# Optimization experiments

Measured on AMD Instinct MI355X. Metric: run time of the kernel, lower is better.

Reference implementation:

```python
import math
import jax, jax.numpy as jnp
import numpy as np

B, T, C, H = 4, 2048, 1024, 16
D = C // H  # head dim = 64


def setup_inputs() -> dict:
    key = jax.random.key(0)
    ks = jax.random.split(key, 5)
    s = 0.02  # trunc_normal-like init scale
    return {
        "x":  jax.random.normal(ks[0], (B, T, C), dtype=jnp.float32),
        "wq": jax.random.normal(ks[1], (C, C), dtype=jnp.float32) * s,
        "bq": jnp.zeros((C,), dtype=jnp.float32),
        "wk": jax.random.normal(ks[2], (C, C), dtype=jnp.float32) * s,
        "bk": jnp.zeros((C,), dtype=jnp.float32),
        "wv": jax.random.normal(ks[3], (C, C), dtype=jnp.float32) * s,
        "bv": jnp.zeros((C,), dtype=jnp.float32),
        "wp": jax.random.normal(ks[4], (C, C), dtype=jnp.float32) * s,
        "bp": jnp.zeros((C,), dtype=jnp.float32),
    }


def reference(x, wq, bq, wk, bk, wv, bv, wp, bp):
    b, t, c = x.shape
    # QKV projections -> (B, H, T, D)
    q = (x @ wq + bq).reshape(b, t, H, D).transpose(0, 2, 1, 3)
    k = (x @ wk + bk).reshape(b, t, H, D).transpose(0, 2, 1, 3)
    v = (x @ wv + bv).reshape(b, t, H, D).transpose(0, 2, 1, 3)
    present = jnp.stack((k, v))  # (2, B, H, T, D)
    # scaled dot-product with causal mask (layer_past is None path)
    att = jnp.einsum('bhqd,bhkd->bhqk', q, k) * (1.0 / math.sqrt(D))
    causal = jnp.tril(jnp.ones((t, t), dtype=bool))  # (T, T)
    att = jnp.where(causal[None, None], att, -jnp.inf)
    att = jax.nn.softmax(att, axis=-1)
    # dropout prob = 0.0 (eval) -> identity
    y = jnp.einsum('bhqk,bhkd->bhqd', att, v)
    y = y.transpose(0, 2, 1, 3).reshape(b, t, c)
    y = y @ wp + bp
    return (y, present)
```

## Files before the change

### kernel.cpp

```cpp
#include <hip/hip_runtime.h>
#include <hip/hip_bf16.h>
#include <stdint.h>

typedef unsigned short u16;
typedef __bf16 bf16x8 __attribute__((ext_vector_type(8)));
typedef __bf16 bf16x4 __attribute__((ext_vector_type(4)));
typedef float f32x4 __attribute__((ext_vector_type(4)));

#define BB 4
#define TT 2048
#define CC 1024
#define HH 16
#define DD 64

#define QSCALE 0.18033688011112042f

__device__ __forceinline__ u16 f2bf(float f) {
  union { float f; unsigned int u; } v; v.f = f;
  unsigned int u = v.u;
  unsigned int r = (u + 0x7fffu + ((u >> 16) & 1u)) >> 16;
  return (u16)r;
}

__device__ __forceinline__ void async_copy16(const void* g, void* l) {
  __builtin_amdgcn_global_load_lds(
      (const __attribute__((address_space(1))) void*)g,
      (__attribute__((address_space(3))) void*)l, 16, 0, 0);
}

__global__ __launch_bounds__(256) void k_cast_x(const float* __restrict__ x,
                                                u16* __restrict__ xb) {
  int i = (blockIdx.x * 256 + threadIdx.x) * 4;
  float4 f = *reinterpret_cast<const float4*>(x + i);
  ushort4 o;
  o.x = f2bf(f.x); o.y = f2bf(f.y); o.z = f2bf(f.z); o.w = f2bf(f.w);
  *reinterpret_cast<ushort4*>(xb + i) = o;
}

__global__ __launch_bounds__(256) void k_transpose_w(
    const float* __restrict__ w0, const float* __restrict__ w1,
    const float* __restrict__ w2, const float* __restrict__ w3,
    u16* __restrict__ t0, u16* __restrict__ t1,
    u16* __restrict__ t2, u16* __restrict__ t3) {
  const float* w = blockIdx.z == 0 ? w0 : blockIdx.z == 1 ? w1 : blockIdx.z == 2 ? w2 : w3;
  u16* t = blockIdx.z == 0 ? t0 : blockIdx.z == 1 ? t1 : blockIdx.z == 2 ? t2 : t3;
  __shared__ u16 tile[32][33];
  int tx = threadIdx.x, ty = threadIdx.y;
  int k0 = blockIdx.x * 32, n0 = blockIdx.y * 32;
#pragma unroll
  for (int r = 0; r < 4; r++)
    tile[ty + r * 8][tx] = f2bf(w[(size_t)(k0 + ty + r * 8) * CC + n0 + tx]);
  __syncthreads();
#pragma unroll
  for (int r = 0; r < 4; r++)
    t[(size_t)(n0 + ty + r * 8) * CC + k0 + tx] = tile[tx][ty + r * 8];
}

__global__ __launch_bounds__(256) void k_transpose_v(
    const float* __restrict__ out_v, u16* __restrict__ vbt) {
  int tb = blockIdx.x * 64;
  int bh = blockIdx.y;
  const float* src = out_v + (size_t)bh * TT * DD;
  u16* dst = vbt + (size_t)bh * TT * DD;
  __shared__ u16 tile[64][65];
  int tid = threadIdx.x;
#pragma unroll
  for (int p = 0; p < 4; p++) {
    int c = p * 256 + tid;
    int t = c >> 4, d0 = (c & 15) * 4;
    float4 f = *reinterpret_cast<const float4*>(src + (size_t)(tb + t) * DD + d0);
    tile[t][d0 + 0] = f2bf(f.x);
    tile[t][d0 + 1] = f2bf(f.y);
    tile[t][d0 + 2] = f2bf(f.z);
    tile[t][d0 + 3] = f2bf(f.w);
  }
  __syncthreads();
#pragma unroll
  for (int p = 0; p < 2; p++) {
    int c = p * 256 + tid;
    int d = c >> 3, t0 = (c & 7) * 8;
    ushort4 lo, hi;
    lo.x = tile[t0 + 0][d]; lo.y = tile[t0 + 1][d];
    lo.z = tile[t0 + 2][d]; lo.w = tile[t0 + 3][d];
    hi.x = tile[t0 + 4][d]; hi.y = tile[t0 + 5][d];
    hi.z = tile[t0 + 6][d]; hi.w = tile[t0 + 7][d];
    u16* o = dst + (size_t)d * TT + tb + t0;
    *reinterpret_cast<ushort4*>(o) = lo;
    *reinterpret_cast<ushort4*>(o + 4) = hi;
  }
}

#define GEMM_PROLOGUE()                                                        \
  int tid = threadIdx.x;                                                       \
  int lane = tid & 63;                                                         \
  int wave = tid >> 6;                                                         \
  int l15 = lane & 15, quad = lane >> 4;                                       \
  int wave_m = wave & 1, wave_n = wave >> 1;                                   \
  __shared__ u16 lA[3][128 * 32];                                              \
  __shared__ u16 lB[3][128 * 32];                                              \
  f32x4 acc[4][4] = {};                                                        \
  int s_c0 = tid, s_c1 = tid + 256;                                            \
  int s_r0 = s_c0 >> 2, s_e0 = ((s_c0 & 3) ^ ((s_c0 >> 3) & 3)) * 8;           \
  int s_r1 = s_c1 >> 2, s_e1 = ((s_c1 & 3) ^ ((s_c1 >> 3) & 3)) * 8;           \
  auto gstage = [&](int buf, int k0) {                                         \
    async_copy16(A + (size_t)(tile_m + s_r0) * CC + k0 + s_e0,                 \
                 &lA[buf][s_c0 * 8]);                                          \
    async_copy16(A + (size_t)(tile_m + s_r1) * CC + k0 + s_e1,                 \
                 &lA[buf][s_c1 * 8]);                                          \
    async_copy16(Bt + (size_t)(tile_n + s_r0) * CC + k0 + s_e0,                \
                 &lB[buf][s_c0 * 8]);                                          \
    async_copy16(Bt + (size_t)(tile_n + s_r1) * CC + k0 + s_e1,                \
                 &lB[buf][s_c1 * 8]);                                          \
  };                                                                           \
  int offA[4], offB[4];                                                        \
  _Pragma("unroll")                                                            \
  for (int i = 0; i < 4; i++) {                                                \
    int rA = wave_m * 64 + i * 16 + l15;                                       \
    offA[i] = rA * 32 + (quad ^ ((rA >> 1) & 3)) * 8;                          \
    int rB = wave_n * 64 + i * 16 + l15;                                       \
    offB[i] = rB * 32 + (quad ^ ((rB >> 1) & 3)) * 8;                          \
  }                                                                            \
  gstage(0, 0);                                                                \
  gstage(1, 32);                                                               \
  int curb = 0;                                                                \
  for (int ks = 0; ks < CC / 32; ks++) {                                       \
    int nxt = curb + 2; nxt = (nxt >= 3) ? nxt - 3 : nxt;                      \
    if (ks < CC / 32 - 2) {                                                    \
      gstage(nxt, (ks + 2) * 32);                                              \
      asm volatile("s_waitcnt vmcnt(8)" ::: "memory");                         \
    } else if (ks == CC / 32 - 2) {                                            \
      asm volatile("s_waitcnt vmcnt(4)" ::: "memory");                         \
    } else {                                                                   \
      asm volatile("s_waitcnt vmcnt(0)" ::: "memory");                         \
    }                                                                          \
    __builtin_amdgcn_sched_barrier(0);                                         \
    __builtin_amdgcn_s_barrier();                                              \
    __builtin_amdgcn_sched_barrier(0);                                         \
    bf16x8 af[4], bfr[4];                                                      \
    _Pragma("unroll")                                                          \
    for (int i = 0; i < 4; i++)                                                \
      af[i] = *reinterpret_cast<const bf16x8*>(&lA[curb][offA[i]]);            \
    _Pragma("unroll")                                                          \
    for (int j = 0; j < 4; j++)                                                \
      bfr[j] = *reinterpret_cast<const bf16x8*>(&lB[curb][offB[j]]);           \
    __builtin_amdgcn_s_setprio(1);                                             \
    _Pragma("unroll")                                                          \
    for (int i = 0; i < 4; i++)                                                \
      _Pragma("unroll")                                                        \
      for (int j = 0; j < 4; j++)                                              \
        acc[i][j] =                                                            \
            __builtin_amdgcn_mfma_f32_16x16x32_bf16(af[i], bfr[j], acc[i][j],  \
                                                    0, 0, 0);                  \
    __builtin_amdgcn_s_setprio(0);                                             \
    __builtin_amdgcn_sched_barrier(0);                                         \
    __builtin_amdgcn_s_barrier();                                              \
    curb = (curb == 2) ? 0 : curb + 1;                                         \
  }

__global__ __launch_bounds__(256) void k_gemm_qkv(
    const u16* __restrict__ xb,
    const u16* __restrict__ wtq, const u16* __restrict__ wtk, const u16* __restrict__ wtv,
    const float* __restrict__ bq, const float* __restrict__ bk, const float* __restrict__ bv,
    u16* __restrict__ qb, u16* __restrict__ kb,
    float* __restrict__ out_k, float* __restrict__ out_v) {
  int mat = blockIdx.z;
  const u16* A = xb;
  const u16* Bt = mat == 0 ? wtq : mat == 1 ? wtk : wtv;
  const float* bias = mat == 0 ? bq : mat == 1 ? bk : bv;
  int tile_m = blockIdx.x * 128;
  int tile_n = blockIdx.y * 128;

  GEMM_PROLOGUE()

#pragma unroll
  for (int j = 0; j < 4; j++) {
    int n = tile_n + wave_n * 64 + j * 16 + l15;
    int h = n >> 6, d = n & 63;
    float bias_n = bias[n];
#pragma unroll
    for (int i = 0; i < 4; i++) {
#pragma unroll
      for (int r = 0; r < 4; r++) {
        int m = tile_m + wave_m * 64 + i * 16 + quad * 4 + r;
        int b = m >> 11, t = m & 2047;
        float val = acc[i][j][r] + bias_n;
        size_t idx = (((size_t)(b * HH + h)) * TT + t) * DD + d;
        if (mat == 0) {
          qb[idx] = f2bf(val * QSCALE);
        } else if (mat == 1) {
          out_k[idx] = val;
          kb[idx] = f2bf(val);
        } else {
          out_v[idx] = val;
        }
      }
    }
  }
}

__global__ __launch_bounds__(256) void k_gemm_proj(
    const u16* __restrict__ yb, const u16* __restrict__ wtp,
    const float* __restrict__ bp, float* __restrict__ out) {
  const u16* A = yb;
  const u16* Bt = wtp;
  int tile_m = blockIdx.x * 128;
  int tile_n = blockIdx.y * 128;

  GEMM_PROLOGUE()

#pragma unroll
  for (int j = 0; j < 4; j++) {
    int n = tile_n + wave_n * 64 + j * 16 + l15;
    float bias_n = bp[n];
#pragma unroll
    for (int i = 0; i < 4; i++) {
#pragma unroll
      for (int r = 0; r < 4; r++) {
        int m = tile_m + wave_m * 64 + i * 16 + quad * 4 + r;
        out[(size_t)m * CC + n] = acc[i][j][r] + bias_n;
      }
    }
  }
}

__global__ __launch_bounds__(256) void k_attn(
    const u16* __restrict__ qb, const u16* __restrict__ kbuf,
    const u16* __restrict__ vtb, u16* __restrict__ yatt) {
  int qpair = blockIdx.x;
  int bh = blockIdx.y;
  int tid = threadIdx.x;
  int lane = tid & 63;
  int wave = tid >> 6;
  int l15 = lane & 15, quad = lane >> 4;

  const u16* Q = qb + (size_t)bh * TT * DD;
  const u16* K = kbuf + (size_t)bh * TT * DD;
  const u16* Vt = vtb + (size_t)bh * TT * DD;

  __shared__ u16 kl[2][64 * 64];
  __shared__ u16 vl[2][64 * 64];
  __shared__ u16 pl[4][16 * 64];
  u16* plw = pl[wave];

  int h = bh & 15, b = bh >> 4;

  int c0 = tid, c1 = tid + 256;
  int r0 = c0 >> 3, e0 = (((c0 & 7) * 16) ^ ((r0 & 7) << 4)) >> 1;
  int r1 = c1 >> 3, e1 = (((c1 & 7) * 16) ^ ((r1 & 7) << 4)) >> 1;

  auto stage = [&](int buf, int kb0) {
    async_copy16(K + (size_t)(kb0 + r0) * DD + e0, &kl[buf][c0 * 8]);
    async_copy16(K + (size_t)(kb0 + r1) * DD + e1, &kl[buf][c1 * 8]);
    async_copy16(Vt + (size_t)r0 * TT + kb0 + e0, &vl[buf][c0 * 8]);
    async_copy16(Vt + (size_t)r1 * TT + kb0 + e1, &vl[buf][c1 * 8]);
  };

  u16* prow = plw + l15 * 64;
  int xrp = (l15 & 7) << 4;
  int q8 = quad << 3;

#pragma unroll
  for (int side = 0; side < 2; side++) {
    int qt = side == 0 ? qpair : 31 - qpair;

    int qr = qt * 64 + wave * 16 + l15;
    bf16x8 qf0 = *reinterpret_cast<const bf16x8*>(Q + (size_t)qr * DD + quad * 8);
    bf16x8 qf1 = *reinterpret_cast<const bf16x8*>(Q + (size_t)qr * DD + 32 + quad * 8);

    f32x4 o_acc[4] = {};
    float m_run = -1e30f, l_run = 0.f;

    stage(0, 0);

    for (int kblk = 0; kblk <= qt; kblk++) {
      int cur = kblk & 1;
      if (kblk < qt) {
        stage(cur ^ 1, (kblk + 1) * 64);
        asm volatile("s_waitcnt vmcnt(4)" ::: "memory");
      } else {
        asm volatile("s_waitcnt vmcnt(0)" ::: "memory");
      }
      __builtin_amdgcn_sched_barrier(0);
      __builtin_amdgcn_s_barrier();
      __builtin_amdgcn_sched_barrier(0);

      f32x4 s_acc[4];
      __builtin_amdgcn_s_setprio(1);
#pragma unroll
      for (int nb = 0; nb < 4; nb++) {
        int krow = nb * 16 + l15;
        int xr = (krow & 7) << 4;
        const u16* kp = &kl[cur][krow * 64];
        bf16x8 kf0 = *reinterpret_cast<const bf16x8*>(kp + (((quad * 16) ^ xr) >> 1));
        bf16x8 kf1 = *reinterpret_cast<const bf16x8*>(kp + (((64 + quad * 16) ^ xr) >> 1));
        f32x4 z = {};
        z = __builtin_amdgcn_mfma_f32_16x16x32_bf16(kf0, qf0, z, 0, 0, 0);
        z = __builtin_amdgcn_mfma_f32_16x16x32_bf16(kf1, qf1, z, 0, 0, 0);
        s_acc[nb] = z;
      }
      __builtin_amdgcn_s_setprio(0);

      float mx = -1e30f;
      if (kblk == qt) {
        int qg = wave * 16 + l15;
#pragma unroll
        for (int nb = 0; nb < 4; nb++)
#pragma unroll
          for (int r = 0; r < 4; r++) {
            int kg = nb * 16 + quad * 4 + r;
            float s = s_acc[nb][r];
            s = (kg <= qg) ? s : -1e30f;
            s_acc[nb][r] = s;
            mx = fmaxf(mx, s);
          }
      } else {
#pragma unroll
        for (int nb = 0; nb < 4; nb++)
#pragma unroll
          for (int r = 0; r < 4; r++) mx = fmaxf(mx, s_acc[nb][r]);
      }
      mx = fmaxf(mx, __shfl_xor(mx, 16, 64));
      mx = fmaxf(mx, __shfl_xor(mx, 32, 64));

      if (!__all(mx - m_run <= 8.0f)) {
        float mnew = fmaxf(m_run, mx);
        float alpha = __builtin_amdgcn_exp2f(m_run - mnew);
        m_run = mnew;
        l_run *= alpha;
        float av[4];
#pragma unroll
        for (int r = 0; r < 4; r++) av[r] = __shfl(alpha, quad * 4 + r, 64);
#pragma unroll
        for (int db = 0; db < 4; db++)
#pragma unroll
          for (int r = 0; r < 4; r++) o_acc[db][r] *= av[r];
      }

      float sum = 0.f;
#pragma unroll
      for (int nb = 0; nb < 4; nb++)
#pragma unroll
        for (int r = 0; r < 4; r++) {
          float e = __builtin_amdgcn_exp2f(s_acc[nb][r] - m_run);
          s_acc[nb][r] = e;
          sum += e;
        }
      sum += __shfl_xor(sum, 16, 64);
      sum += __shfl_xor(sum, 32, 64);
      l_run += sum;

#pragma unroll
      for (int nb = 0; nb < 4; nb++) {
        bf16x4 pk = {(__bf16)s_acc[nb][0], (__bf16)s_acc[nb][1],
                     (__bf16)s_acc[nb][2], (__bf16)s_acc[nb][3]};
        *reinterpret_cast<bf16x4*>(prow + ((((nb << 5) + q8) ^ xrp) >> 1)) = pk;
      }

      __builtin_amdgcn_s_setprio(1);
#pragma unroll
      for (int half = 0; half < 2; half++) {
        bf16x8 pf = *reinterpret_cast<const bf16x8*>(
            prow + (((half * 64 + quad * 16) ^ xrp) >> 1));
#pragma unroll
        for (int db = 0; db < 4; db++) {
          int vrow = db * 16 + l15;
          bf16x8 vf = *reinterpret_cast<const bf16x8*>(
              &vl[cur][vrow * 64] + (((half * 64 + quad * 16) ^ ((vrow & 7) << 4)) >> 1));
          o_acc[db] = __builtin_amdgcn_mfma_f32_16x16x32_bf16(pf, vf, o_acc[db], 0, 0, 0);
        }
      }
      __builtin_amdgcn_s_setprio(0);

      __builtin_amdgcn_sched_barrier(0);
      __builtin_amdgcn_s_barrier();
    }

    float lr[4];
#pragma unroll
    for (int r = 0; r < 4; r++) lr[r] = __shfl(l_run, quad * 4 + r, 64);
#pragma unroll
    for (int r = 0; r < 4; r++) {
      float inv = 1.0f / lr[r];
      int tq = qt * 64 + wave * 16 + quad * 4 + r;
#pragma unroll
      for (int db = 0; db < 4; db++) {
        int d = db * 16 + l15;
        yatt[((size_t)(b * TT + tq)) * CC + h * DD + d] = f2bf(o_acc[db][r] * inv);
      }
    }
  }
}

extern "C" void kernel_launch(void* const* d_in, const int* in_sizes, int n_in,
                              void* d_out, int out_size, void* d_ws, size_t ws_size,
                              hipStream_t stream) {
  const float* x  = (const float*)d_in[0];
  const float* wq = (const float*)d_in[1];
  const float* bq = (const float*)d_in[2];
  const float* wk = (const float*)d_in[3];
  const float* bk = (const float*)d_in[4];
  const float* wv = (const float*)d_in[5];
  const float* bv = (const float*)d_in[6];
  const float* wp = (const float*)d_in[7];
  const float* bp = (const float*)d_in[8];

  float* out_y = (float*)d_out;
  float* out_k = out_y + (size_t)BB * TT * CC;
  float* out_v = out_k + (size_t)BB * HH * TT * DD;

  u16* xb  = (u16*)d_ws;
  u16* wtq = xb + (size_t)BB * TT * CC;
  u16* wtk = wtq + (size_t)CC * CC;
  u16* wtv = wtk + (size_t)CC * CC;
  u16* wtp = wtv + (size_t)CC * CC;
  u16* qb  = wtp + (size_t)CC * CC;
  u16* kb  = qb + (size_t)BB * TT * CC;
  u16* vbt = kb + (size_t)BB * TT * CC;
  u16* yb  = vbt + (size_t)BB * TT * CC;

  k_cast_x<<<(BB * TT * CC) / 1024, 256, 0, stream>>>(x, xb);
  k_transpose_w<<<dim3(CC / 32, CC / 32, 4), dim3(32, 8), 0, stream>>>(
      wq, wk, wv, wp, wtq, wtk, wtv, wtp);
  k_gemm_qkv<<<dim3(BB * TT / 128, CC / 128, 3), 256, 0, stream>>>(
      xb, wtq, wtk, wtv, bq, bk, bv, qb, kb, out_k, out_v);
  k_transpose_v<<<dim3(TT / 64, BB * HH), 256, 0, stream>>>(out_v, vbt);
  k_attn<<<dim3(16, BB * HH), 256, 0, stream>>>(qb, kb, vbt, yb);
  k_gemm_proj<<<dim3(BB * TT / 128, CC / 128), 256, 0, stream>>>(yb, wtp, bp, out_y);
}
```

Measured before the change: 339.6 us.

## Fuse x cast with weight transpose and write transposed V in QKV epilogue

New measurement: 345.0 us. About the same (+1.6%).

```diff
diff --git a/kernel.cpp b/kernel.cpp
--- a/kernel.cpp
+++ b/kernel.cpp
@@ -28,65 +28,34 @@
       (__attribute__((address_space(3))) void*)l, 16, 0, 0);
 }
 
-__global__ __launch_bounds__(256) void k_cast_x(const float* __restrict__ x,
-                                                u16* __restrict__ xb) {
-  int i = (blockIdx.x * 256 + threadIdx.x) * 4;
-  float4 f = *reinterpret_cast<const float4*>(x + i);
-  ushort4 o;
-  o.x = f2bf(f.x); o.y = f2bf(f.y); o.z = f2bf(f.z); o.w = f2bf(f.w);
-  *reinterpret_cast<ushort4*>(xb + i) = o;
-}
-
-__global__ __launch_bounds__(256) void k_transpose_w(
+__global__ __launch_bounds__(256) void k_prep(
+    const float* __restrict__ x, u16* __restrict__ xb,
     const float* __restrict__ w0, const float* __restrict__ w1,
     const float* __restrict__ w2, const float* __restrict__ w3,
     u16* __restrict__ t0, u16* __restrict__ t1,
     u16* __restrict__ t2, u16* __restrict__ t3) {
-  const float* w = blockIdx.z == 0 ? w0 : blockIdx.z == 1 ? w1 : blockIdx.z == 2 ? w2 : w3;
-  u16* t = blockIdx.z == 0 ? t0 : blockIdx.z == 1 ? t1 : blockIdx.z == 2 ? t2 : t3;
-  __shared__ u16 tile[32][33];
+  int z = blockIdx.z;
   int tx = threadIdx.x, ty = threadIdx.y;
-  int k0 = blockIdx.x * 32, n0 = blockIdx.y * 32;
-#pragma unroll
-  for (int r = 0; r < 4; r++)
-    tile[ty + r * 8][tx] = f2bf(w[(size_t)(k0 + ty + r * 8) * CC + n0 + tx]);
-  __syncthreads();
-#pragma unroll
-  for (int r = 0; r < 4; r++)
-    t[(size_t)(n0 + ty + r * 8) * CC + k0 + tx] = tile[tx][ty + r * 8];
-}
-
-__global__ __launch_bounds__(256) void k_transpose_v(
-    const float* __restrict__ out_v, u16* __restrict__ vbt) {
-  int tb = blockIdx.x * 64;
-  int bh = blockIdx.y;
-  const float* src = out_v + (size_t)bh * TT * DD;
-  u16* dst = vbt + (size_t)bh * TT * DD;
-  __shared__ u16 tile[64][65];
-  int tid = threadIdx.x;
-#pragma unroll
-  for (int p = 0; p < 4; p++) {
-    int c = p * 256 + tid;
-    int t = c >> 4, d0 = (c & 15) * 4;
-    float4 f = *reinterpret_cast<const float4*>(src + (size_t)(tb + t) * DD + d0);
-    tile[t][d0 + 0] = f2bf(f.x);
-    tile[t][d0 + 1] = f2bf(f.y);
-    tile[t][d0 + 2] = f2bf(f.z);
-    tile[t][d0 + 3] = f2bf(f.w);
-  }
-  __syncthreads();
-#pragma unroll
-  for (int p = 0; p < 2; p++) {
-    int c = p * 256 + tid;
-    int d = c >> 3, t0 = (c & 7) * 8;
-    ushort4 lo, hi;
-    lo.x = tile[t0 + 0][d]; lo.y = tile[t0 + 1][d];
-    lo.z = tile[t0 + 2][d]; lo.w = tile[t0 + 3][d];
-    hi.x = tile[t0 + 4][d]; hi.y = tile[t0 + 5][d];
-    hi.z = tile[t0 + 6][d]; hi.w = tile[t0 + 7][d];
-    u16* o = dst + (size_t)d * TT + tb + t0;
-    *reinterpret_cast<ushort4*>(o) = lo;
-    *reinterpret_cast<ushort4*>(o + 4) = hi;
+  if (z < 4) {
+    const float* w = z == 0 ? w0 : z == 1 ? w1 : z == 2 ? w2 : w3;
+    u16* t = z == 0 ? t0 : z == 1 ? t1 : z == 2 ? t2 : t3;
+    __shared__ u16 tile[32][33];
+    int k0 = blockIdx.x * 32, n0 = blockIdx.y * 32;
+#pragma unroll
+    for (int r = 0; r < 4; r++)
+      tile[ty + r * 8][tx] = f2bf(w[(size_t)(k0 + ty + r * 8) * CC + n0 + tx]);
+    __syncthreads();
+#pragma unroll
+    for (int r = 0; r < 4; r++)
+      t[(size_t)(n0 + ty + r * 8) * CC + k0 + tx] = tile[tx][ty + r * 8];
+  } else {
+    int bid = (z - 4) * 1024 + blockIdx.y * 32 + blockIdx.x;
+    int tid = ty * 32 + tx;
+    int i = (bid * 256 + tid) * 4;
+    float4 f = *reinterpret_cast<const float4*>(x + i);
+    ushort4 o;
+    o.x = f2bf(f.x); o.y = f2bf(f.y); o.z = f2bf(f.z); o.w = f2bf(f.w);
+    *reinterpret_cast<ushort4*>(xb + i) = o;
   }
 }
 
@@ -161,7 +130,7 @@
     const u16* __restrict__ xb,
     const u16* __restrict__ wtq, const u16* __restrict__ wtk, const u16* __restrict__ wtv,
     const float* __restrict__ bq, const float* __restrict__ bk, const float* __restrict__ bv,
-    u16* __restrict__ qb, u16* __restrict__ kb,
+    u16* __restrict__ qb, u16* __restrict__ kb, u16* __restrict__ vbt,
     float* __restrict__ out_k, float* __restrict__ out_v) {
   int mat = blockIdx.z;
   const u16* A = xb;
@@ -179,19 +148,34 @@
     float bias_n = bias[n];
 #pragma unroll
     for (int i = 0; i < 4; i++) {
-#pragma unroll
-      for (int r = 0; r < 4; r++) {
-        int m = tile_m + wave_m * 64 + i * 16 + quad * 4 + r;
-        int b = m >> 11, t = m & 2047;
-        float val = acc[i][j][r] + bias_n;
-        size_t idx = (((size_t)(b * HH + h)) * TT + t) * DD + d;
-        if (mat == 0) {
-          qb[idx] = f2bf(val * QSCALE);
-        } else if (mat == 1) {
-          out_k[idx] = val;
-          kb[idx] = f2bf(val);
-        } else {
-          out_v[idx] = val;
+      if (mat == 2) {
+        float v4[4];
+        int t0g = tile_m + wave_m * 64 + i * 16 + quad * 4;
+        int b0 = t0g >> 11, tt = t0g & 2047;
+#pragma unroll
+        for (int r = 0; r < 4; r++) {
+          float val = acc[i][j][r] + bias_n;
+          v4[r] = val;
+          out_v[(((size_t)(b0 * HH + h)) * TT + tt + r) * DD + d] = val;
+        }
+        ushort4 pk;
+        pk.x = f2bf(v4[0]); pk.y = f2bf(v4[1]);
+        pk.z = f2bf(v4[2]); pk.w = f2bf(v4[3]);
+        *reinterpret_cast<ushort4*>(
+            vbt + ((size_t)(b0 * HH + h) * DD + d) * TT + tt) = pk;
+      } else {
+#pragma unroll
+        for (int r = 0; r < 4; r++) {
+          int m = tile_m + wave_m * 64 + i * 16 + quad * 4 + r;
+          int b = m >> 11, t = m & 2047;
+          float val = acc[i][j][r] + bias_n;
+          size_t idx = (((size_t)(b * HH + h)) * TT + t) * DD + d;
+          if (mat == 0) {
+            qb[idx] = f2bf(val * QSCALE);
+          } else {
+            out_k[idx] = val;
+            kb[idx] = f2bf(val);
+          }
         }
       }
     }
@@ -418,12 +402,10 @@
   u16* vbt = kb + (size_t)BB * TT * CC;
   u16* yb  = vbt + (size_t)BB * TT * CC;
 
-  k_cast_x<<<(BB * TT * CC) / 1024, 256, 0, stream>>>(x, xb);
-  k_transpose_w<<<dim3(CC / 32, CC / 32, 4), dim3(32, 8), 0, stream>>>(
-      wq, wk, wv, wp, wtq, wtk, wtv, wtp);
+  k_prep<<<dim3(32, 32, 12), dim3(32, 8), 0, stream>>>(
+      x, xb, wq, wk, wv, wp, wtq, wtk, wtv, wtp);
   k_gemm_qkv<<<dim3(BB * TT / 128, CC / 128, 3), 256, 0, stream>>>(
-      xb, wtq, wtk, wtv, bq, bk, bv, qb, kb, out_k, out_v);
-  k_transpose_v<<<dim3(TT / 64, BB * HH), 256, 0, stream>>>(out_v, vbt);
+      xb, wtq, wtk, wtv, bq, bk, bv, qb, kb, vbt, out_k, out_v);
   k_attn<<<dim3(16, BB * HH), 256, 0, stream>>>(qb, kb, vbt, yb);
   k_gemm_proj<<<dim3(BB * TT / 128, CC / 128), 256, 0, stream>>>(yb, wtp, bp, out_y);
 }
```
